# Optimization experiments

Hardware: AMD Instinct MI355X
Metric: run time of the kernel (lower is better)

The kernel has to match this reference:

```python
import jax, jax.numpy as jnp
import numpy as np

NEG_SLOPE = 0.2


def _gat_conv(x, src, dst, W, a_src, a_dst, b, n_nodes):
    # Single-head PyG GATConv (normalize arg in source is ignored by GATConv).
    h = x @ W                                   # [N, C_out]
    e_src = h @ a_src                           # [N] alpha_src contribution
    e_dst = h @ a_dst                           # [N] alpha_dst contribution
    logits = jax.nn.leaky_relu(e_src[src] + e_dst[dst], NEG_SLOPE)  # [E]
    m = jax.ops.segment_max(logits, dst, num_segments=n_nodes)      # per-dst max
    e = jnp.exp(logits - m[dst])
    denom = jax.ops.segment_sum(e, dst, num_segments=n_nodes)
    alpha = e / denom[dst]                      # edge softmax over in-neighbors
    out = jax.ops.segment_sum(h[src] * alpha[:, None], dst, num_segments=n_nodes)
    return out + b


def _add_self_loops(edge_index, n_nodes):
    loop = jnp.arange(n_nodes, dtype=edge_index.dtype)
    src = jnp.concatenate([edge_index[0], loop])
    dst = jnp.concatenate([edge_index[1], loop])
    return src, dst


def setup_inputs() -> dict:
    key = jax.random.key(0)
    ks = jax.random.split(key, 16)
    N, E, C_IN, C_HID, C_OUT = 50000, 1600000, 128, 128, 64
    x = jax.random.normal(ks[0], (N, C_IN), dtype=jnp.float32)
    edge_index = jax.random.randint(ks[1], (2, E), 0, N, dtype=jnp.int32)
    glorot = lambda k, shape: jax.random.normal(k, shape, jnp.float32) * np.sqrt(2.0 / sum(shape))
    return {
        "x": x,
        "edge_index": edge_index,
        "W0": glorot(ks[2], (C_IN, C_HID)),
        "as0": glorot(ks[3], (C_HID,)) * 0.1,
        "ad0": glorot(ks[4], (C_HID,)) * 0.1,
        "b0": jnp.zeros((C_HID,), jnp.float32),
        "W1": glorot(ks[5], (C_HID, C_HID)),
        "as1": glorot(ks[6], (C_HID,)) * 0.1,
        "ad1": glorot(ks[7], (C_HID,)) * 0.1,
        "b1": jnp.zeros((C_HID,), jnp.float32),
        "W2": glorot(ks[8], (C_HID, C_OUT)),
        "as2": glorot(ks[9], (C_OUT,)) * 0.1,
        "ad2": glorot(ks[10], (C_OUT,)) * 0.1,
        "b2": jnp.zeros((C_OUT,), jnp.float32),
    }


def reference(x, edge_index, W0, as0, ad0, b0, W1, as1, ad1, b1, W2, as2, ad2, b2):
    n_nodes = x.shape[0]
    src, dst = _add_self_loops(edge_index, n_nodes)
    # eval mode: F.dropout with training=False is identity
    h = jax.nn.relu(_gat_conv(x, src, dst, W0, as0, ad0, b0, n_nodes))
    h = jax.nn.relu(_gat_conv(h, src, dst, W1, as1, ad1, b1, n_nodes))
    out = _gat_conv(h, src, dst, W2, as2, ad2, b2, n_nodes)
    return out
```

## Files before the change

kernel.cpp:

```cpp
#include <hip/hip_runtime.h>
#include <hip/hip_bf16.h>
#include <type_traits>

#define DEVFN __device__ __forceinline__

typedef __attribute__((ext_vector_type(8))) short bfrag;
typedef __attribute__((ext_vector_type(4))) float facc4;

DEVFN float lrelu(float v) { return (v >= 0.f) ? v : 0.2f * v; }

DEVFN float2 bf2x2(unsigned u) {
  return make_float2(__uint_as_float(u << 16), __uint_as_float(u & 0xFFFF0000u));
}
DEVFN float bf1(unsigned short b) { return __uint_as_float(((unsigned)b) << 16); }
DEVFN unsigned short f2bf(float f) {
  __hip_bfloat16 h = __float2bfloat16(f);
  return *reinterpret_cast<unsigned short*>(&h);
}
DEVFN unsigned packbf2(float x, float y) {
  return (unsigned)f2bf(x) | ((unsigned)f2bf(y) << 16);
}

DEVFN float wave_sum(float v) {
#pragma unroll
  for (int o = 1; o < 64; o <<= 1) v += __shfl_xor(v, o, 64);
  return v;
}
DEVFN float wave_max(float v) {
#pragma unroll
  for (int o = 1; o < 64; o <<= 1) v = fmaxf(v, __shfl_xor(v, o, 64));
  return v;
}

template<int C, bool A_FP32>
__global__ __launch_bounds__(256) void gemm_mfma(const void* __restrict__ Xin,
                                                 const float* __restrict__ W,
                                                 const float* __restrict__ a_src,
                                                 const float* __restrict__ a_dst,
                                                 unsigned short* __restrict__ H,
                                                 float* __restrict__ es,
                                                 float* __restrict__ ed,
                                                 int N) {
  constexpr int K = 128;
  constexpr int LSTR = K + 8;
  constexpr int NT = C / 16;
  __shared__ unsigned short WsT[C * LSTR];

  const int t = threadIdx.x;
  for (int i = t; i < K * C; i += 256) {
    int k = i / C;
    int c = i - k * C;
    WsT[c * LSTR + k] = f2bf(W[i]);
  }
  __syncthreads();

  const int wave = t >> 6;
  const int lane = t & 63;
  const int l15 = lane & 15;
  const int quad = lane >> 4;
  const int arow = blockIdx.x * 64 + wave * 16 + l15;
  const bool avalid = arow < N;

  facc4 acc[NT];
#pragma unroll
  for (int i = 0; i < NT; ++i) acc[i] = (facc4){0.f, 0.f, 0.f, 0.f};

#pragma unroll
  for (int ks = 0; ks < 4; ++ks) {
    bfrag a;
    if (A_FP32) {
      if (avalid) {
        const float* xp = (const float*)Xin + (size_t)arow * K + quad * 8 + ks * 32;
        float4 u = *(const float4*)xp;
        float4 v = *(const float4*)(xp + 4);
        a[0] = (short)f2bf(u.x); a[1] = (short)f2bf(u.y);
        a[2] = (short)f2bf(u.z); a[3] = (short)f2bf(u.w);
        a[4] = (short)f2bf(v.x); a[5] = (short)f2bf(v.y);
        a[6] = (short)f2bf(v.z); a[7] = (short)f2bf(v.w);
      } else {
        a = (bfrag){0, 0, 0, 0, 0, 0, 0, 0};
      }
    } else {
      const unsigned short* xp =
          (const unsigned short*)Xin + (size_t)arow * K + quad * 8 + ks * 32;
      a = *(const bfrag*)xp;
    }
#pragma unroll
    for (int ct = 0; ct < NT; ++ct) {
      bfrag b = *(const bfrag*)(&WsT[(ct * 16 + l15) * LSTR + ks * 32 + quad * 8]);
      acc[ct] = __builtin_amdgcn_mfma_f32_16x16x32_bf16(a, b, acc[ct], 0, 0, 0);
    }
  }

  float asv[NT], adv[NT];
#pragma unroll
  for (int ct = 0; ct < NT; ++ct) {
    asv[ct] = a_src[ct * 16 + l15];
    adv[ct] = a_dst[ct * 16 + l15];
  }

  const int orow0 = blockIdx.x * 64 + wave * 16 + quad * 4;
#pragma unroll
  for (int r = 0; r < 4; ++r) {
    const int orow = orow0 + r;
    float ps = 0.f, pd = 0.f;
#pragma unroll
    for (int ct = 0; ct < NT; ++ct) {
      if (orow < N) H[(size_t)orow * C + ct * 16 + l15] = f2bf(acc[ct][r]);
      ps += acc[ct][r] * asv[ct];
      pd += acc[ct][r] * adv[ct];
    }
#pragma unroll
    for (int msk = 1; msk < 16; msk <<= 1) {
      ps += __shfl_xor(ps, msk, 64);
      pd += __shfl_xor(pd, msk, 64);
    }
    if (l15 == 0 && orow < N) { es[orow] = ps; ed[orow] = pd; }
  }
}

__global__ void hist_deg(const int* __restrict__ dst, int* __restrict__ deg,
                         int* __restrict__ hmat, int E, int nbk, int chunk) {
  __shared__ int hist[128];
  const int t = threadIdx.x;
  if (t < nbk) hist[t] = 0;
  __syncthreads();
  const int e0 = blockIdx.x * chunk;
  const int e1 = min(E, e0 + chunk);
  for (int e = e0 + t; e < e1; e += 256) {
    int d = dst[e];
    atomicAdd(deg + d, 1);
    atomicAdd(&hist[d >> 9], 1);
  }
  __syncthreads();
  if (t < nbk) hmat[t * gridDim.x + blockIdx.x] = hist[t];
}

__global__ void scan_partial(const int* __restrict__ in, int* __restrict__ csum, int n) {
  __shared__ int sh[256];
  int i = blockIdx.x * 256 + threadIdx.x;
  sh[threadIdx.x] = (i < n) ? in[i] : 0;
  __syncthreads();
  for (int o = 128; o > 0; o >>= 1) {
    if (threadIdx.x < o) sh[threadIdx.x] += sh[threadIdx.x + o];
    __syncthreads();
  }
  if (threadIdx.x == 0) csum[blockIdx.x] = sh[0];
}

__global__ void scan_chunks(int* __restrict__ csum, int nch) {
  __shared__ int sh[256];
  __shared__ int carry;
  if (threadIdx.x == 0) carry = 0;
  __syncthreads();
  for (int base = 0; base < nch; base += 256) {
    int i = base + threadIdx.x;
    int v = (i < nch) ? csum[i] : 0;
    sh[threadIdx.x] = v;
    __syncthreads();
    for (int o = 1; o < 256; o <<= 1) {
      int t = (threadIdx.x >= o) ? sh[threadIdx.x - o] : 0;
      __syncthreads();
      sh[threadIdx.x] += t;
      __syncthreads();
    }
    if (i < nch) csum[i] = carry + sh[threadIdx.x] - v;
    __syncthreads();
    if (threadIdx.x == 255) carry += sh[255];
    __syncthreads();
  }
}

__global__ void scan_final(const int* __restrict__ deg, const int* __restrict__ csum,
                           int* __restrict__ rp, int* __restrict__ wp, int N, int E) {
  __shared__ int sh[256];
  int i = blockIdx.x * 256 + threadIdx.x;
  int v = (i < N) ? deg[i] : 0;
  sh[threadIdx.x] = v;
  __syncthreads();
  for (int o = 1; o < 256; o <<= 1) {
    int t = (threadIdx.x >= o) ? sh[threadIdx.x - o] : 0;
    __syncthreads();
    sh[threadIdx.x] += t;
    __syncthreads();
  }
  if (i < N) {
    int r = csum[blockIdx.x] + sh[threadIdx.x] - v;
    rp[i] = r;
    wp[i] = r;
  }
  if (blockIdx.x == 0 && threadIdx.x == 0) rp[N] = E;
}

__global__ void scan_final_excl(const int* __restrict__ in, const int* __restrict__ csum,
                                int* __restrict__ out, int n) {
  __shared__ int sh[256];
  int i = blockIdx.x * 256 + threadIdx.x;
  int v = (i < n) ? in[i] : 0;
  sh[threadIdx.x] = v;
  __syncthreads();
  for (int o = 1; o < 256; o <<= 1) {
    int t = (threadIdx.x >= o) ? sh[threadIdx.x - o] : 0;
    __syncthreads();
    sh[threadIdx.x] += t;
    __syncthreads();
  }
  if (i < n) out[i] = csum[blockIdx.x] + sh[threadIdx.x] - v;
}

__global__ void place_pass(const int* __restrict__ src, const int* __restrict__ dst,
                           const int* __restrict__ off, int2* __restrict__ be,
                           int E, int nbk, int chunk) {
  __shared__ int cur[128];
  const int t = threadIdx.x;
  if (t < nbk) cur[t] = off[t * gridDim.x + blockIdx.x];
  __syncthreads();
  const int e0 = blockIdx.x * chunk;
  const int e1 = min(E, e0 + chunk);
  for (int e = e0 + t; e < e1; e += 256) {
    int d = dst[e];
    int s = src[e];
    int p = atomicAdd(&cur[d >> 9], 1);
    be[p] = make_int2(s, d);
  }
}

__global__ void bucket_final(const int2* __restrict__ be, const int* __restrict__ off,
                             const int* __restrict__ rp, unsigned short* __restrict__ col,
                             int E, int N, int nbk, int pblk) {
  __shared__ int cur[512];
  const int b = blockIdx.x;
  const int n0 = b << 9;
  const int cnt = min(512, N - n0);
  const int t = threadIdx.x;
  for (int i = t; i < cnt; i += 256) cur[i] = rp[n0 + i];
  __syncthreads();
  const int e0 = off[b * pblk];
  const int e1 = (b + 1 < nbk) ? off[(b + 1) * pblk] : E;
  for (int e = e0 + t; e < e1; e += 256) {
    int2 sd = be[e];
    int p = atomicAdd(&cur[sd.y - n0], 1);
    col[p] = (unsigned short)sd.x;
  }
}

__global__ void csr_scatter_ranged(const int* __restrict__ src,
                                   const int* __restrict__ dst,
                                   int* __restrict__ wp, int* __restrict__ col,
                                   int E, int range, int npass) {
  const int stride = gridDim.x * blockDim.x;
  const int gid = blockIdx.x * blockDim.x + threadIdx.x;
  for (int pass = 0; pass < npass; ++pass) {
    const int lo = pass * range;
    const int hi = lo + range;
    for (int e = gid; e < E; e += stride) {
      int d = dst[e];
      if (d >= lo && d < hi) {
        int p = atomicAdd(wp + d, 1);
        col[p] = src[e];
      }
    }
  }
}

__global__ void csr_count(const int* __restrict__ dst, int* __restrict__ deg, int E) {
  int e = blockIdx.x * blockDim.x + threadIdx.x;
  if (e < E) atomicAdd(deg + dst[e], 1);
}

template<bool RELU, bool OUT_BF16, typename IT>
__global__ void gat_fused128(const int* __restrict__ row_ptr,
                             const IT* __restrict__ col,
                             const float* __restrict__ es,
                             const float* __restrict__ ed,
                             const unsigned short* __restrict__ H,
                             const float* __restrict__ bias,
                             void* __restrict__ outX, int N) {
  const int lane = threadIdx.x & 63;
  const int n = blockIdx.x * (blockDim.x >> 6) + (threadIdx.x >> 6);
  if (n >= N) return;

  const int k0 = row_ptr[n];
  const int k1 = row_ptr[n + 1];
  const int deg = k1 - k0;
  const float edd = ed[n];
  const float self_lg = lrelu(es[n] + edd);

  const unsigned* Hp = (const unsigned*)H;
  float ax0 = 0.f, ay0 = 0.f, ax1 = 0.f, ay1 = 0.f;
  float den, sp;

  if (deg <= 64) {
    int k = k0 + lane;
    bool act = (k < k1);
    int c = act ? (int)col[k] : 0;
    float lg = act ? lrelu(es[c] + edd) : -3.0e38f;
    float m = fmaxf(wave_max(lg), self_lg);
    float p = act ? __expf(lg - m) : 0.f;
    sp = __expf(self_lg - m);
    den = wave_sum(p) + sp;
    int j = 0;
    for (; j + 8 <= deg; j += 8) {
      int ss[8];
      float pp[8];
      unsigned uu[8];
#pragma unroll
      for (int q = 0; q < 8; ++q) {
        ss[q] = __shfl(c, j + q);
        pp[q] = __shfl(p, j + q);
      }
#pragma unroll
      for (int q = 0; q < 8; ++q) uu[q] = Hp[(size_t)ss[q] * 64 + lane];
#pragma unroll
      for (int q = 0; q < 8; ++q) {
        float2 h = bf2x2(uu[q]);
        if (q & 1) { ax1 += pp[q] * h.x; ay1 += pp[q] * h.y; }
        else       { ax0 += pp[q] * h.x; ay0 += pp[q] * h.y; }
      }
    }
    for (; j < deg; ++j) {
      int s = __shfl(c, j);
      float pj = __shfl(p, j);
      float2 h = bf2x2(Hp[(size_t)s * 64 + lane]);
      ax0 += pj * h.x; ay0 += pj * h.y;
    }
  } else {
    float mloc = self_lg;
    for (int base = k0; base < k1; base += 64) {
      int k = base + lane;
      if (k < k1) mloc = fmaxf(mloc, lrelu(es[(int)col[k]] + edd));
    }
    float m = wave_max(mloc);
    sp = __expf(self_lg - m);
    den = sp;
    for (int base = k0; base < k1; base += 64) {
      int k = base + lane;
      bool act = (k < k1);
      int c = act ? (int)col[k] : 0;
      float p = act ? __expf(lrelu(es[c] + edd) - m) : 0.f;
      den += wave_sum(p);
      int len = min(64, k1 - base);
      for (int j = 0; j < len; ++j) {
        int s = __shfl(c, j);
        float pj = __shfl(p, j);
        float2 h = bf2x2(Hp[(size_t)s * 64 + lane]);
        ax0 += pj * h.x; ay0 += pj * h.y;
      }
    }
  }

  float2 hv = bf2x2(Hp[(size_t)n * 64 + lane]);
  ax0 += sp * hv.x; ay0 += sp * hv.y;
  float inv = 1.f / den;
  float2 bv = ((const float2*)bias)[lane];
  float vx = (ax0 + ax1) * inv + bv.x;
  float vy = (ay0 + ay1) * inv + bv.y;
  if (RELU) { vx = fmaxf(vx, 0.f); vy = fmaxf(vy, 0.f); }
  if (OUT_BF16)
    ((unsigned*)outX)[(size_t)n * 64 + lane] = packbf2(vx, vy);
  else
    ((float2*)outX)[(size_t)n * 64 + lane] = make_float2(vx, vy);
}

template<bool RELU, typename IT>
__global__ void gat_fused64(const int* __restrict__ row_ptr,
                            const IT* __restrict__ col,
                            const float* __restrict__ es,
                            const float* __restrict__ ed,
                            const unsigned short* __restrict__ H,
                            const float* __restrict__ bias,
                            float* __restrict__ outX, int N) {
  const int lane = threadIdx.x & 63;
  const int n = blockIdx.x * (blockDim.x >> 6) + (threadIdx.x >> 6);
  if (n >= N) return;

  const int k0 = row_ptr[n];
  const int k1 = row_ptr[n + 1];
  const int deg = k1 - k0;
  const float edd = ed[n];
  const float self_lg = lrelu(es[n] + edd);

  float a0 = 0.f, a1 = 0.f;
  float den, sp;

  if (deg <= 64) {
    int k = k0 + lane;
    bool act = (k < k1);
    int c = act ? (int)col[k] : 0;
    float lg = act ? lrelu(es[c] + edd) : -3.0e38f;
    float m = fmaxf(wave_max(lg), self_lg);
    float p = act ? __expf(lg - m) : 0.f;
    sp = __expf(self_lg - m);
    den = wave_sum(p) + sp;
    int j = 0;
    for (; j + 8 <= deg; j += 8) {
      int ss[8];
      float pp[8];
      unsigned short uu[8];
#pragma unroll
      for (int q = 0; q < 8; ++q) {
        ss[q] = __shfl(c, j + q);
        pp[q] = __shfl(p, j + q);
      }
#pragma unroll
      for (int q = 0; q < 8; ++q) uu[q] = H[(size_t)ss[q] * 64 + lane];
#pragma unroll
      for (int q = 0; q < 8; ++q) {
        if (q & 1) a1 += pp[q] * bf1(uu[q]);
        else       a0 += pp[q] * bf1(uu[q]);
      }
    }
    for (; j < deg; ++j) {
      int s = __shfl(c, j);
      float pj = __shfl(p, j);
      a0 += pj * bf1(H[(size_t)s * 64 + lane]);
    }
  } else {
    float mloc = self_lg;
    for (int base = k0; base < k1; base += 64) {
      int k = base + lane;
      if (k < k1) mloc = fmaxf(mloc, lrelu(es[(int)col[k]] + edd));
    }
    float m = wave_max(mloc);
    sp = __expf(self_lg - m);
    den = sp;
    for (int base = k0; base < k1; base += 64) {
      int k = base + lane;
      bool act = (k < k1);
      int c = act ? (int)col[k] : 0;
      float p = act ? __expf(lrelu(es[c] + edd) - m) : 0.f;
      den += wave_sum(p);
      int len = min(64, k1 - base);
      for (int j = 0; j < len; ++j) {
        int s = __shfl(c, j);
        float pj = __shfl(p, j);
        a0 += pj * bf1(H[(size_t)s * 64 + lane]);
      }
    }
  }

  a0 += sp * bf1(H[(size_t)n * 64 + lane]);
  float v = (a0 + a1) / den + bias[lane];
  if (RELU) v = fmaxf(v, 0.f);
  outX[(size_t)n * 64 + lane] = v;
}


extern "C" void kernel_launch(void* const* d_in, const int* in_sizes, int n_in,
                              void* d_out, int out_size, void* d_ws, size_t ws_size,
                              hipStream_t stream) {
  const int C_HID = in_sizes[3];
  const int C_FIN = in_sizes[11];
  const int C_IN  = in_sizes[2] / C_HID;
  const int N     = in_sizes[0] / C_IN;
  const int E     = in_sizes[1] / 2;
  const int NPAD  = ((N + 63) / 64) * 64;

  const float* x = (const float*)d_in[0];
  const int* ei  = (const int*)d_in[1];
  const int* src = ei;
  const int* dst = ei + E;

  const float* W0  = (const float*)d_in[2];
  const float* as0 = (const float*)d_in[3];
  const float* ad0 = (const float*)d_in[4];
  const float* b0  = (const float*)d_in[5];
  const float* W1  = (const float*)d_in[6];
  const float* as1 = (const float*)d_in[7];
  const float* ad1 = (const float*)d_in[8];
  const float* b1  = (const float*)d_in[9];
  const float* W2  = (const float*)d_in[10];
  const float* as2 = (const float*)d_in[11];
  const float* ad2 = (const float*)d_in[12];
  const float* b2  = (const float*)d_in[13];

  char* base = (char*)d_ws;
  size_t off = 0;
  auto alloc = [&](size_t bytes) -> char* {
    char* p = base + off;
    off = (off + bytes + 255) & ~((size_t)255);
    return p;
  };
  const int PBLK = 512;
  const int NBK  = (N + 511) >> 9;
  const int M    = NBK * PBLK;
  const int NCH  = (N + 255) / 256;
  const int MCH  = (M + 255) / 256;
  const int SCH  = (NCH > MCH ? NCH : MCH);

  unsigned short* XB  = (unsigned short*)alloc((size_t)NPAD * C_HID * 2);
  unsigned short* H   = (unsigned short*)alloc((size_t)N * C_HID * 2);
  float* ES    = (float*)alloc((size_t)N * sizeof(float));
  float* ED    = (float*)alloc((size_t)N * sizeof(float));
  int*   RP    = (int*)alloc((size_t)(N + 1) * sizeof(int));
  int*   WP    = (int*)alloc((size_t)N * sizeof(int));
  void*  COL   = (void*)alloc((size_t)E * sizeof(int));
  int*   DEG   = (int*)alloc((size_t)N * sizeof(int));
  int*   CSUM  = (int*)alloc((size_t)SCH * sizeof(int));
  int*   HMAT  = (int*)alloc((size_t)M * sizeof(int));
  int*   OFF   = (int*)alloc((size_t)M * sizeof(int));
  int2*  BE    = (int2*)alloc((size_t)E * sizeof(int2));
  (void)ws_size;

  const int wgrid = (N + 3) / 4;
  const int mgrid = NPAD / 64;
  const bool u16 = (N <= 65535);

  hipMemsetAsync(DEG, 0, (size_t)N * sizeof(int), stream);
  if (u16) {
    const int CHUNK = (E + PBLK - 1) / PBLK;
    hist_deg<<<PBLK, 256, 0, stream>>>(dst, DEG, HMAT, E, NBK, CHUNK);
    scan_partial<<<NCH, 256, 0, stream>>>(DEG, CSUM, N);
    scan_chunks<<<1, 256, 0, stream>>>(CSUM, NCH);
    scan_final<<<NCH, 256, 0, stream>>>(DEG, CSUM, RP, WP, N, E);
    scan_partial<<<MCH, 256, 0, stream>>>(HMAT, CSUM, M);
    scan_chunks<<<1, 256, 0, stream>>>(CSUM, MCH);
    scan_final_excl<<<MCH, 256, 0, stream>>>(HMAT, CSUM, OFF, M);
    place_pass<<<PBLK, 256, 0, stream>>>(src, dst, OFF, BE, E, NBK, CHUNK);
    bucket_final<<<NBK, 256, 0, stream>>>(BE, OFF, RP, (unsigned short*)COL,
                                          E, N, NBK, PBLK);
  } else {
    const int ET256 = (E + 255) / 256;
    csr_count<<<ET256, 256, 0, stream>>>(dst, DEG, E);
    scan_partial<<<NCH, 256, 0, stream>>>(DEG, CSUM, N);
    scan_chunks<<<1, 256, 0, stream>>>(CSUM, NCH);
    scan_final<<<NCH, 256, 0, stream>>>(DEG, CSUM, RP, WP, N, E);
    const int NPASS = 8;
    const int range = (N + NPASS - 1) / NPASS;
    csr_scatter_ranged<<<2048, 256, 0, stream>>>(src, dst, WP, (int*)COL, E,
                                                 range, NPASS);
  }

  auto run_layers = [&](auto* col) {
    using IT = typename std::remove_pointer<decltype(col)>::type;
    gemm_mfma<128, true><<<mgrid, 256, 0, stream>>>(x, W0, as0, ad0, H, ES, ED, N);
    gat_fused128<true, true, IT><<<wgrid, 256, 0, stream>>>(RP, col, ES, ED, H, b0, XB, N);
    gemm_mfma<128, false><<<mgrid, 256, 0, stream>>>(XB, W1, as1, ad1, H, ES, ED, N);
    gat_fused128<true, true, IT><<<wgrid, 256, 0, stream>>>(RP, col, ES, ED, H, b1, XB, N);
    gemm_mfma<64, false><<<mgrid, 256, 0, stream>>>(XB, W2, as2, ad2, H, ES, ED, N);
    gat_fused64<false, IT><<<wgrid, 256, 0, stream>>>(RP, col, ES, ED, H, b2,
                                                      (float*)d_out, N);
  };

  if (u16) run_layers((unsigned short*)COL);
  else     run_layers((int*)COL);
  (void)out_size; (void)n_in;
}
```

Measured before the change: 408.5 us.

## Derive per-node CSR offsets inside bucket kernel, drop global degree atomics

Removes the per-edge global atomic degree count, the memset and the three-kernel node-degree scan from the bucketed CSR build. Each bucket block now counts its nodes' in-degrees in shared memory from the bucketed edge pairs, runs a local prefix scan, and writes the row pointers itself. The bucket histogram is also split into four per-wave copies to reduce shared atomic contention. In exchange, each bucket block reads its edge list twice, and every block performs a serial block-wide scan.

```diff
diff --git a/kernel.cpp b/kernel.cpp
--- a/kernel.cpp
+++ b/kernel.cpp
@@ -119,21 +119,22 @@
   }
 }
 
-__global__ void hist_deg(const int* __restrict__ dst, int* __restrict__ deg,
-                         int* __restrict__ hmat, int E, int nbk, int chunk) {
-  __shared__ int hist[128];
+__global__ void hist_only(const int* __restrict__ dst, int* __restrict__ hmat,
+                          int E, int nbk, int chunk) {
+  __shared__ int hist[4 * 128];
   const int t = threadIdx.x;
-  if (t < nbk) hist[t] = 0;
-  __syncthreads();
+  for (int i = t; i < 4 * 128; i += 256) hist[i] = 0;
+  __syncthreads();
+  int* h = &hist[(t >> 6) << 7];
   const int e0 = blockIdx.x * chunk;
   const int e1 = min(E, e0 + chunk);
   for (int e = e0 + t; e < e1; e += 256) {
-    int d = dst[e];
-    atomicAdd(deg + d, 1);
-    atomicAdd(&hist[d >> 9], 1);
-  }
-  __syncthreads();
-  if (t < nbk) hmat[t * gridDim.x + blockIdx.x] = hist[t];
+    atomicAdd(&h[dst[e] >> 9], 1);
+  }
+  __syncthreads();
+  if (t < nbk)
+    hmat[t * gridDim.x + blockIdx.x] =
+        hist[t] + hist[t + 128] + hist[t + 256] + hist[t + 384];
 }
 
 __global__ void scan_partial(const int* __restrict__ in, int* __restrict__ csum, int n) {
@@ -226,17 +227,39 @@
 }
 
 __global__ void bucket_final(const int2* __restrict__ be, const int* __restrict__ off,
-                             const int* __restrict__ rp, unsigned short* __restrict__ col,
+                             int* __restrict__ rp, unsigned short* __restrict__ col,
                              int E, int N, int nbk, int pblk) {
   __shared__ int cur[512];
+  __shared__ int ps[256];
   const int b = blockIdx.x;
   const int n0 = b << 9;
   const int cnt = min(512, N - n0);
   const int t = threadIdx.x;
-  for (int i = t; i < cnt; i += 256) cur[i] = rp[n0 + i];
+  for (int i = t; i < cnt; i += 256) cur[i] = 0;
   __syncthreads();
   const int e0 = off[b * pblk];
   const int e1 = (b + 1 < nbk) ? off[(b + 1) * pblk] : E;
+  for (int e = e0 + t; e < e1; e += 256) {
+    int2 sd = be[e];
+    atomicAdd(&cur[sd.y - n0], 1);
+  }
+  __syncthreads();
+  const int i0 = 2 * t, i1 = 2 * t + 1;
+  const int v0 = (i0 < cnt) ? cur[i0] : 0;
+  const int v1 = (i1 < cnt) ? cur[i1] : 0;
+  ps[t] = v0 + v1;
+  __syncthreads();
+  for (int o = 1; o < 256; o <<= 1) {
+    int u = (t >= o) ? ps[t - o] : 0;
+    __syncthreads();
+    ps[t] += u;
+    __syncthreads();
+  }
+  const int base = e0 + ps[t] - (v0 + v1);
+  if (i0 < cnt) { rp[n0 + i0] = base;      cur[i0] = base; }
+  if (i1 < cnt) { rp[n0 + i1] = base + v0; cur[i1] = base + v0; }
+  if (b == nbk - 1 && t == 0) rp[N] = E;
+  __syncthreads();
   for (int e = e0 + t; e < e1; e += 256) {
     int2 sd = be[e];
     int p = atomicAdd(&cur[sd.y - n0], 1);
@@ -506,13 +529,9 @@
   const int mgrid = NPAD / 64;
   const bool u16 = (N <= 65535);
 
-  hipMemsetAsync(DEG, 0, (size_t)N * sizeof(int), stream);
   if (u16) {
     const int CHUNK = (E + PBLK - 1) / PBLK;
-    hist_deg<<<PBLK, 256, 0, stream>>>(dst, DEG, HMAT, E, NBK, CHUNK);
-    scan_partial<<<NCH, 256, 0, stream>>>(DEG, CSUM, N);
-    scan_chunks<<<1, 256, 0, stream>>>(CSUM, NCH);
-    scan_final<<<NCH, 256, 0, stream>>>(DEG, CSUM, RP, WP, N, E);
+    hist_only<<<PBLK, 256, 0, stream>>>(dst, HMAT, E, NBK, CHUNK);
     scan_partial<<<MCH, 256, 0, stream>>>(HMAT, CSUM, M);
     scan_chunks<<<1, 256, 0, stream>>>(CSUM, MCH);
     scan_final_excl<<<MCH, 256, 0, stream>>>(HMAT, CSUM, OFF, M);
@@ -520,6 +539,7 @@
     bucket_final<<<NBK, 256, 0, stream>>>(BE, OFF, RP, (unsigned short*)COL,
                                           E, N, NBK, PBLK);
   } else {
+    hipMemsetAsync(DEG, 0, (size_t)N * sizeof(int), stream);
     const int ET256 = (E + 255) / 256;
     csr_count<<<ET256, 256, 0, stream>>>(dst, DEG, E);
     scan_partial<<<NCH, 256, 0, stream>>>(DEG, CSUM, N);
```

New measurement: 346.7 us. 1.18x faster.
